# Kernel tuning notes

Measured on AMD Instinct MI355X. Metric: run time of the kernel, lower is better.

## Reference

```python
import jax, jax.numpy as jnp
import numpy as np
from jax import lax

N, CIN, COUT, T, V, S = 64, 64, 64, 256, 25, 3
REL = CIN // 8  # 8, per __init__ branch for in_channels=64


def setup_inputs() -> dict:
    key = jax.random.key(0)
    ks = jax.random.split(key, 22)
    rn = lambda i, shape, s=0.05: jax.random.normal(ks[i], shape, jnp.float32) * s
    return dict(
        x=jax.random.normal(ks[0], (N, CIN, T, V), jnp.float32),
        A=rn(1, (S, V, V), 0.2),                 # adaptive PA parameter
        alpha=jnp.asarray(0.1, jnp.float32),     # unit_gcn alpha (scalar)
        w1=rn(2, (S, REL, CIN)), b1=rn(3, (S, REL)),
        w2=rn(4, (S, REL, CIN)), b2=rn(5, (S, REL)),
        w3=rn(6, (S, COUT, CIN)), b3=rn(7, (S, COUT)),
        w4=rn(8, (S, COUT, REL)), b4=rn(9, (S, COUT)),
        pm_w1=rn(10, (S, REL, 2 * REL)), pm_b1=rn(11, (S, REL)),
        pm_w2=rn(12, (S, REL, REL)), pm_b2=rn(13, (S, REL)),
        dw_w=rn(14, (S, REL, 1, 3, 3)),          # depthwise 3x3, groups=REL
        proj_w=rn(15, (S, COUT, REL)),           # aux_proj, no bias
        beta=rn(16, (S,), 0.01), gamma=rn(17, (S,), 0.01),
        bn_w=jnp.ones((COUT,), jnp.float32), bn_b=jnp.zeros((COUT,), jnp.float32),
    )


def _sorgc(x, Ai, alpha, w1, b1, w2, b2, w3, b3, w4, b4,
           pw1, pb1, pw2, pb2, dww, pjw, beta, gamma):
    # x: (N, C, T, V)
    xm = x.mean(axis=2)                                            # (N,C,V) -- 1x1 conv is linear, so conv then mean == mean then conv
    x1 = jnp.einsum('ncv,rc->nrv', xm, w1) + b1[:, None]           # (N,R,V)
    x2 = jnp.einsum('ncv,rc->nrv', xm, w2) + b2[:, None]
    x3 = jnp.einsum('nctv,oc->notv', x, w3) + b3[:, None, None]    # (N,O,T,V)
    q1 = jnp.tanh(x1[:, :, :, None] - x2[:, :, None, :])           # (N,R,V,V)
    psi = jnp.broadcast_to(x2[:, :, :, None], q1.shape)
    phi = jnp.broadcast_to(x2[:, :, None, :], q1.shape)
    pair = jnp.concatenate([psi, phi], axis=1)                     # (N,2R,V,V)
    h = jax.nn.relu(jnp.einsum('npuv,rp->nruv', pair, pw1) + pb1[:, None, None])
    q2 = jnp.einsum('npuv,rp->nruv', h, pw2) + pb2[:, None, None]
    q_all = q1 + gamma * q2
    R = (jnp.einsum('nruv,or->nouv', q_all, w4) + b4[:, None, None]) * alpha + Ai[None, None]
    # aux branch: depthwise 3x3 conv -> avgpool3x3 (count_include_pad) -> tanh -> 1x1 proj
    Ra = lax.conv_general_dilated(q1, dww, (1, 1), [(1, 1), (1, 1)],
                                  dimension_numbers=('NCHW', 'OIHW', 'NCHW'),
                                  feature_group_count=q1.shape[1])
    Ra = lax.reduce_window(Ra, 0.0, lax.add, (1, 1, 3, 3), (1, 1, 1, 1),
                           [(0, 0), (0, 0), (1, 1), (1, 1)]) / 9.0
    Ra = jnp.tanh(Ra)
    Ra = jnp.einsum('nruv,or->nouv', Ra, pjw)                      # (N,O,V,V)
    R = R + beta * Ra
    return jnp.einsum('ncuv,nctv->nctu', R, x3)                    # (N,O,T,V)


def reference(x, A, alpha, w1, b1, w2, b2, w3, b3, w4, b4,
              pm_w1, pm_b1, pm_w2, pm_b2, dw_w, proj_w, beta, gamma, bn_w, bn_b):
    y = None
    for i in range(S):
        z = _sorgc(x, A[i], alpha, w1[i], b1[i], w2[i], b2[i], w3[i], b3[i],
                   w4[i], b4[i], pm_w1[i], pm_b1[i], pm_w2[i], pm_b2[i],
                   dw_w[i], proj_w[i], beta[i], gamma[i])
        y = z if y is None else y + z
    # BatchNorm2d (training-mode batch statistics), eps=1e-5
    mu = y.mean(axis=(0, 2, 3), keepdims=True)
    var = y.var(axis=(0, 2, 3), keepdims=True)
    y = (y - mu) * lax.rsqrt(var + 1e-5) * bn_w[None, :, None, None] + bn_b[None, :, None, None]
    y = y + x  # residual (in_channels == out_channels -> identity down)
    return jax.nn.relu(y)
```

## Files before the change

### kernel.cpp

```cpp
#include <hip/hip_runtime.h>


#define WS_R_BYTE   409600

typedef __attribute__((ext_vector_type(8))) short bf16x8;
typedef __attribute__((ext_vector_type(4))) float f32x4;

typedef __attribute__((address_space(1))) unsigned int uint_g;
typedef __attribute__((address_space(3))) unsigned int uint_l;

static __device__ __forceinline__ unsigned short f2bf(float f) {
    unsigned int u = __float_as_uint(f);
    u += 0x7fff + ((u >> 16) & 1);
    return (unsigned short)(u >> 16);
}
static __device__ __forceinline__ float bf2f(unsigned short s) {
    return __uint_as_float(((unsigned int)s) << 16);
}
static __device__ __forceinline__ void gload_lds16(const void* g, void* l) {
    __builtin_amdgcn_global_load_lds((const uint_g*)g, (uint_l*)l, 16, 0, 0);
}

__global__ __launch_bounds__(256) void k_xm(const float* __restrict__ x,
                                            float* __restrict__ ws) {
    __shared__ float sm[6400];
    __shared__ float part[200];
    const int tid = threadIdx.x;
    const int n = blockIdx.x >> 6, c = blockIdx.x & 63;
    const float4* p = (const float4*)(x + (unsigned)(n * 64 + c) * 6400u);
    float4* s4 = (float4*)sm;
    for (int i = tid; i < 1600; i += 256) s4[i] = p[i];
    __syncthreads();
    if (tid < 200) {
        int v = tid % 25, g = tid / 25;
        float s = 0.f;
        for (int tt = 0; tt < 32; tt++) s += sm[(g * 32 + tt) * 25 + v];
        part[tid] = s;
    }
    __syncthreads();
    if (tid < 25) {
        float s = 0.f;
        #pragma unroll
        for (int g = 0; g < 8; g++) s += part[g * 25 + tid];
        ws[n * 1600 + c * 25 + tid] = s * (1.f / 256.f);
    }
}

__global__ __launch_bounds__(512) void k_small(
    const float* __restrict__ ws, unsigned short* __restrict__ Rg,
    const float* __restrict__ A, const float* __restrict__ alphap,
    const float* __restrict__ w1, const float* __restrict__ b1,
    const float* __restrict__ w2, const float* __restrict__ b2,
    const float* __restrict__ w4, const float* __restrict__ b4,
    const float* __restrict__ pw1, const float* __restrict__ pb1,
    const float* __restrict__ pw2, const float* __restrict__ pb2,
    const float* __restrict__ dww, const float* __restrict__ pjw,
    const float* __restrict__ beta, const float* __restrict__ gamma) {
    __shared__ float sm[15000];
    const int tid = threadIdx.x;
    const int s = blockIdx.x >> 6;
    const int n = blockIdx.x & 63;
    const float alpha = alphap[0];
    const float gam = gamma[s], bet = beta[s];

    for (int i = tid; i < 1600; i += 512) sm[5000 + i] = ws[n * 1600 + i];
    __syncthreads();

    for (int i = tid; i < 400; i += 512) {
        int half = i / 200, j = i % 200;
        int r = j / 25, k = j % 25;
        const float* w = (half ? w2 : w1) + (s * 8 + r) * 64;
        float acc = (half ? b2 : b1)[s * 8 + r];
        for (int c = 0; c < 64; c++) acc += w[c] * sm[5000 + c * 25 + k];
        sm[6600 + i] = acc;
    }
    __syncthreads();

    for (int i = tid; i < 5400; i += 512) {
        if (i < 5000) {
            int r = i / 625, uv = i % 625, u = uv / 25, v = uv % 25;
            sm[i] = tanhf(sm[6600 + r * 25 + u] - sm[6800 + r * 25 + v]);
        } else {
            int i2 = i - 5000;
            int half = i2 / 200, j = i2 % 200;
            int r = j / 25, k = j % 25;
            float acc = 0.f;
            for (int p = 0; p < 8; p++)
                acc += pw1[(s * 8 + r) * 16 + half * 8 + p] * sm[6800 + p * 25 + k];
            sm[7000 + i2] = acc;
        }
    }
    __syncthreads();

    for (int i = tid; i < 5000; i += 512) {
        int r = i / 625, uv = i % 625, u = uv / 25, v = uv % 25;
        float t = sm[7000 + r * 25 + u] + sm[7200 + r * 25 + v] + pb1[s * 8 + r];
        sm[10000 + i] = t > 0.f ? t : 0.f;
    }
    __syncthreads();

    for (int i = tid; i < 5000; i += 512) {
        int r = i / 625, uv = i % 625;
        float q2 = pb2[s * 8 + r];
        for (int p = 0; p < 8; p++)
            q2 += pw2[(s * 8 + r) * 8 + p] * sm[10000 + p * 625 + uv];
        sm[5000 + i] = sm[i] + gam * q2;
    }
    __syncthreads();

    for (int i = tid; i < 5000; i += 512) {
        int r = i / 625, uv = i % 625, u = uv / 25, v = uv % 25;
        float acc = 0.f;
        for (int di = 0; di < 3; di++) {
            int uu = u + di - 1;
            if (uu < 0 || uu > 24) continue;
            for (int dj = 0; dj < 3; dj++) {
                int vv = v + dj - 1;
                if (vv < 0 || vv > 24) continue;
                acc += sm[r * 625 + uu * 25 + vv] * dww[(s * 8 + r) * 9 + di * 3 + dj];
            }
        }
        sm[10000 + i] = acc;
    }
    __syncthreads();

    for (int i = tid; i < 5000; i += 512) {
        int r = i / 625, uv = i % 625, u = uv / 25, v = uv % 25;
        float acc = 0.f;
        for (int di = 0; di < 3; di++) {
            int uu = u + di - 1;
            if (uu < 0 || uu > 24) continue;
            for (int dj = 0; dj < 3; dj++) {
                int vv = v + dj - 1;
                if (vv < 0 || vv > 24) continue;
                acc += sm[10000 + r * 625 + uu * 25 + vv];
            }
        }
        sm[i] = tanhf(acc * (1.f / 9.f));
    }
    __syncthreads();

    unsigned short* Rb = Rg + (unsigned)(s * 64 + n) * 44800u;
    for (int i = tid; i < 44800; i += 512) {
        int o, vv, uu;
        if (i < 43008) {
            int vg = i / 5376, rem = i % 5376;
            o = rem / 84;
            int j = rem % 84;
            vv = vg * 3 + j / 28;
            uu = j % 28;
        } else {
            int rem = i - 43008;
            o = rem / 28;
            vv = 24;
            uu = rem % 28;
        }
        unsigned short val = 0;
        if (uu < 25) {
            int quv = uu * 25 + vv;
            float mn = b4[s * 64 + o], aux = 0.f;
            for (int r = 0; r < 8; r++) {
                mn  += w4[(s * 64 + o) * 8 + r] * sm[5000 + r * 625 + quv];
                aux += pjw[(s * 64 + o) * 8 + r] * sm[r * 625 + quv];
            }
            val = f2bf(mn * alpha + A[s * 625 + quv] + bet * aux);
        }
        Rb[i] = val;
    }
}

__global__ __launch_bounds__(256, 2) void k_main(
    const float* __restrict__ x, const float* __restrict__ w3,
    const float* __restrict__ b3, const unsigned short* __restrict__ Rg,
    float* __restrict__ out, float* __restrict__ bnacc) {
    __shared__ __align__(16) unsigned char smem[73728];
    unsigned short* xb = (unsigned short*)smem;
    unsigned char* RsBase = smem + 51200;

    const int tid  = threadIdx.x;
    const int blk  = ((int)blockIdx.x & 7) * 128 + ((int)blockIdx.x >> 3);
    const int n    = blk >> 4;
    const int t0   = (blk & 15) * 16;
    const int lane = tid & 63;
    const int w    = tid >> 6;
    const int ln15 = lane & 15;
    const int q    = lane >> 4;
    const int og   = w * 16 + ln15;

    const unsigned short* Rn0 = Rg;

    {
        const char* src = (const char*)Rg + (size_t)((0 * 64 + n) * 44800) * 2;
        unsigned char* dst = RsBase;
        for (int j = w; j < 11; j += 4)
            gload_lds16(src + j * 1024 + (lane << 4), dst + j * 1024);
    }

    {
        const float* xbase = x + n * 409600 + t0 * 25;
        #pragma unroll 5
        for (int k = 0; k < 25; k++) {
            int i  = tid + k * 256;
            int tv = i % 400;
            int cq = i / 400;
            const float* p = xbase + cq * 4 * 6400 + tv;
            ushort4 h;
            h.x = f2bf(p[0]); h.y = f2bf(p[6400]);
            h.z = f2bf(p[12800]); h.w = f2bf(p[19200]);
            int addr = tv * 64 + (((cq >> 1) ^ (tv & 7)) << 3) + ((cq & 1) << 2);
            *(ushort4*)&xb[addr] = h;
        }
    }
    __syncthreads();

    float yacc[25][4];
    #pragma unroll
    for (int u = 0; u < 25; u++)
        #pragma unroll
        for (int r = 0; r < 4; r++) yacc[u][r] = 0.f;

    int buf = 0;
    for (int s = 0; s < 3; s++) {
        bf16x8 bfr[2];
        {
            const float* wp = w3 + (s * 64 + og) * 64;
            #pragma unroll
            for (int ks = 0; ks < 2; ks++)
                #pragma unroll
                for (int j = 0; j < 8; j++)
                    bfr[ks][j] = (short)f2bf(wp[ks * 32 + q * 8 + j]);
        }
        const float bias = b3[s * 64 + og];

        for (int vg = 0; vg < 9; vg++) {
            {
                int ns = s, nvg = vg + 1;
                if (nvg == 9) { ns = s + 1; nvg = 0; }
                if (ns < 3) {
                    const char* src = (const char*)Rg +
                        (size_t)((ns * 64 + n) * 44800 + nvg * 5376) * 2;
                    unsigned char* dst = RsBase + (buf ^ 1) * 11264;
                    const int rounds = (nvg < 8) ? 11 : 4;
                    for (int j = w; j < rounds; j += 4)
                        gload_lds16(src + j * 1024 + (lane << 4), dst + j * 1024);
                }
            }

            const unsigned short* RsB = (const unsigned short*)(RsBase + buf * 11264);
            const int nv = (vg < 8) ? 3 : 1;

            f32x4 c[3];
            #pragma unroll
            for (int iv = 0; iv < 3; iv++) {
                if (iv >= nv) break;
                const int v   = vg * 3 + iv;
                const int row = ln15 * 25 + v;
                const int sw  = row & 7;
                bf16x8 a0 = *(const bf16x8*)&xb[row * 64 + ((q ^ sw) << 3)];
                bf16x8 a1 = *(const bf16x8*)&xb[row * 64 + (((4 + q) ^ sw) << 3)];
                f32x4 cc; cc[0] = bias; cc[1] = bias; cc[2] = bias; cc[3] = bias;
                cc = __builtin_amdgcn_mfma_f32_16x16x32_bf16(a0, bfr[0], cc, 0, 0, 0);
                cc = __builtin_amdgcn_mfma_f32_16x16x32_bf16(a1, bfr[1], cc, 0, 0, 0);
                c[iv] = cc;
            }
            #pragma unroll
            for (int iv = 0; iv < 3; iv++) {
                if (iv >= nv) break;
                const unsigned short* rr = (vg < 8) ? &RsB[og * 84 + iv * 28]
                                                    : &RsB[og * 28];
                f32x4 cc = c[iv];
                #pragma unroll
                for (int ug = 0; ug < 6; ug++) {
                    ushort4 r4 = *(const ushort4*)(rr + ug * 4);
                    float f0 = bf2f(r4.x), f1 = bf2f(r4.y);
                    float f2 = bf2f(r4.z), f3 = bf2f(r4.w);
                    #pragma unroll
                    for (int r = 0; r < 4; r++) {
                        yacc[ug * 4 + 0][r] += f0 * cc[r];
                        yacc[ug * 4 + 1][r] += f1 * cc[r];
                        yacc[ug * 4 + 2][r] += f2 * cc[r];
                        yacc[ug * 4 + 3][r] += f3 * cc[r];
                    }
                }
                float f24 = bf2f(rr[24]);
                #pragma unroll
                for (int r = 0; r < 4; r++) yacc[24][r] += f24 * cc[r];
            }

            __syncthreads();
            buf ^= 1;
        }
    }

    float* op = out + (n * 64 + og) * 6400 + t0 * 25;
    float s1 = 0.f, s2 = 0.f;
    #pragma unroll
    for (int r = 0; r < 4; r++) {
        float* opr = op + (q * 4 + r) * 25;
        #pragma unroll
        for (int u = 0; u < 25; u++) {
            float vv = yacc[u][r];
            opr[u] = vv;
            s1 += vv; s2 += vv * vv;
        }
    }
    s1 += __shfl_xor(s1, 16); s1 += __shfl_xor(s1, 32);
    s2 += __shfl_xor(s2, 16); s2 += __shfl_xor(s2, 32);
    if (q == 0) {
        atomicAdd(&bnacc[og * 16], s1);
        atomicAdd(&bnacc[1024 + og * 16], s2);
    }
}

__global__ __launch_bounds__(256) void k_final(
    float* __restrict__ out, const float* __restrict__ x,
    const float* __restrict__ bnacc,
    const float* __restrict__ bnw, const float* __restrict__ bnb) {
    const int idx4 = blockIdx.x * 256 + threadIdx.x;
    const int o = (idx4 / 1600) & 63;
    const float cnt = 1.f / 409600.f;
    float mean = bnacc[o * 16] * cnt;
    float var = bnacc[1024 + o * 16] * cnt - mean * mean;
    float inv = rsqrtf(var + 1e-5f);
    float sc = bnw[o] * inv;
    float sh = bnb[o] - mean * sc;
    float4 y = ((const float4*)out)[idx4];
    float4 xv = ((const float4*)x)[idx4];
    y.x = fmaxf(y.x * sc + sh + xv.x, 0.f);
    y.y = fmaxf(y.y * sc + sh + xv.y, 0.f);
    y.z = fmaxf(y.z * sc + sh + xv.z, 0.f);
    y.w = fmaxf(y.w * sc + sh + xv.w, 0.f);
    ((float4*)out)[idx4] = y;
}

extern "C" void kernel_launch(void* const* d_in, const int* in_sizes, int n_in,
                              void* d_out, int out_size, void* d_ws, size_t ws_size,
                              hipStream_t stream) {
    const float* x     = (const float*)d_in[0];
    const float* A     = (const float*)d_in[1];
    const float* alpha = (const float*)d_in[2];
    const float* w1    = (const float*)d_in[3];
    const float* b1    = (const float*)d_in[4];
    const float* w2    = (const float*)d_in[5];
    const float* b2    = (const float*)d_in[6];
    const float* w3    = (const float*)d_in[7];
    const float* b3    = (const float*)d_in[8];
    const float* w4    = (const float*)d_in[9];
    const float* b4    = (const float*)d_in[10];
    const float* pw1   = (const float*)d_in[11];
    const float* pb1   = (const float*)d_in[12];
    const float* pw2   = (const float*)d_in[13];
    const float* pb2   = (const float*)d_in[14];
    const float* dww   = (const float*)d_in[15];
    const float* pjw   = (const float*)d_in[16];
    const float* beta  = (const float*)d_in[17];
    const float* gamma = (const float*)d_in[18];
    const float* bnw   = (const float*)d_in[19];
    const float* bnb   = (const float*)d_in[20];
    float* out = (float*)d_out;
    float* ws  = (float*)d_ws;
    unsigned short* wsR = (unsigned short*)((char*)d_ws + WS_R_BYTE);
    float* wsBN = ws;

    k_xm<<<4096, 256, 0, stream>>>(x, ws);
    k_small<<<192, 512, 0, stream>>>(ws, wsR, A, alpha, w1, b1, w2, b2,
                                     w4, b4, pw1, pb1, pw2, pb2, dww, pjw,
                                     beta, gamma);
    hipMemsetAsync(wsBN, 0, 8192, stream);
    k_main<<<1024, 256, 0, stream>>>(x, w3, b3, wsR, out, wsBN);
    k_final<<<25600, 256, 0, stream>>>(out, x, wsBN, bnw, bnb);
}
```

Baseline: 434.0 us.

## Merge last v-groups, use packed f32x2 FMAs, fold memset, double k_final work

Several changes at once. The R layout is reorganised so the final v-group covers four columns (21-24) instead of a separate single-column group, which cuts the main-loop iterations and barriers from 9 to 8 per s. The accumulator becomes f32x2 vectors so the compiler can emit packed FMA instructions. The BN accumulator memset moves into k_xm (block 0) at a separate workspace offset, which removes a launch, and k_final processes two float4s per thread. The costs are larger LDS buffers, which may affect occupancy, and a zeroing step that depends on kernel ordering.

```diff
diff --git a/kernel.cpp b/kernel.cpp
--- a/kernel.cpp
+++ b/kernel.cpp
@@ -2,9 +2,11 @@
 
 
 #define WS_R_BYTE   409600
+#define WS_BN_BYTE  17612800
 
 typedef __attribute__((ext_vector_type(8))) short bf16x8;
 typedef __attribute__((ext_vector_type(4))) float f32x4;
+typedef __attribute__((ext_vector_type(2))) float f32x2;
 
 typedef __attribute__((address_space(1))) unsigned int uint_g;
 typedef __attribute__((address_space(3))) unsigned int uint_l;
@@ -22,10 +24,14 @@
 }
 
 __global__ __launch_bounds__(256) void k_xm(const float* __restrict__ x,
-                                            float* __restrict__ ws) {
+                                            float* __restrict__ ws,
+                                            float* __restrict__ bnacc) {
     __shared__ float sm[6400];
     __shared__ float part[200];
     const int tid = threadIdx.x;
+    if (blockIdx.x == 0) {
+        for (int i = tid; i < 2048; i += 256) bnacc[i] = 0.f;
+    }
     const int n = blockIdx.x >> 6, c = blockIdx.x & 63;
     const float4* p = (const float4*)(x + (unsigned)(n * 64 + c) * 6400u);
     float4* s4 = (float4*)sm;
@@ -143,17 +149,18 @@
     unsigned short* Rb = Rg + (unsigned)(s * 64 + n) * 44800u;
     for (int i = tid; i < 44800; i += 512) {
         int o, vv, uu;
-        if (i < 43008) {
+        if (i < 37632) {
             int vg = i / 5376, rem = i % 5376;
             o = rem / 84;
             int j = rem % 84;
             vv = vg * 3 + j / 28;
             uu = j % 28;
         } else {
-            int rem = i - 43008;
-            o = rem / 28;
-            vv = 24;
-            uu = rem % 28;
+            int rem = i - 37632;
+            o = rem / 112;
+            int j = rem % 112;
+            vv = 21 + j / 28;
+            uu = j % 28;
         }
         unsigned short val = 0;
         if (uu < 25) {
@@ -173,7 +180,7 @@
     const float* __restrict__ x, const float* __restrict__ w3,
     const float* __restrict__ b3, const unsigned short* __restrict__ Rg,
     float* __restrict__ out, float* __restrict__ bnacc) {
-    __shared__ __align__(16) unsigned char smem[73728];
+    __shared__ __align__(16) unsigned char smem[79872];
     unsigned short* xb = (unsigned short*)smem;
     unsigned char* RsBase = smem + 51200;
 
@@ -187,10 +194,8 @@
     const int q    = lane >> 4;
     const int og   = w * 16 + ln15;
 
-    const unsigned short* Rn0 = Rg;
-
     {
-        const char* src = (const char*)Rg + (size_t)((0 * 64 + n) * 44800) * 2;
+        const char* src = (const char*)Rg + (size_t)(n * 44800) * 2;
         unsigned char* dst = RsBase;
         for (int j = w; j < 11; j += 4)
             gload_lds16(src + j * 1024 + (lane << 4), dst + j * 1024);
@@ -213,11 +218,12 @@
     }
     __syncthreads();
 
-    float yacc[25][4];
+    f32x2 yacc[25][2];
     #pragma unroll
-    for (int u = 0; u < 25; u++)
-        #pragma unroll
-        for (int r = 0; r < 4; r++) yacc[u][r] = 0.f;
+    for (int u = 0; u < 25; u++) {
+        yacc[u][0] = (f32x2){0.f, 0.f};
+        yacc[u][1] = (f32x2){0.f, 0.f};
+    }
 
     int buf = 0;
     for (int s = 0; s < 3; s++) {
@@ -232,26 +238,27 @@
         }
         const float bias = b3[s * 64 + og];
 
-        for (int vg = 0; vg < 9; vg++) {
+        for (int vg = 0; vg < 8; vg++) {
             {
                 int ns = s, nvg = vg + 1;
-                if (nvg == 9) { ns = s + 1; nvg = 0; }
+                if (nvg == 8) { ns = s + 1; nvg = 0; }
                 if (ns < 3) {
                     const char* src = (const char*)Rg +
                         (size_t)((ns * 64 + n) * 44800 + nvg * 5376) * 2;
-                    unsigned char* dst = RsBase + (buf ^ 1) * 11264;
-                    const int rounds = (nvg < 8) ? 11 : 4;
+                    unsigned char* dst = RsBase + (buf ^ 1) * 14336;
+                    const int rounds = (nvg < 7) ? 11 : 14;
                     for (int j = w; j < rounds; j += 4)
                         gload_lds16(src + j * 1024 + (lane << 4), dst + j * 1024);
                 }
             }
 
-            const unsigned short* RsB = (const unsigned short*)(RsBase + buf * 11264);
-            const int nv = (vg < 8) ? 3 : 1;
-
-            f32x4 c[3];
+            const unsigned short* RsB = (const unsigned short*)(RsBase + buf * 14336);
+            const int nv = (vg < 7) ? 3 : 4;
+            const int rowstride = (vg < 7) ? 84 : 112;
+
+            f32x4 c[4];
             #pragma unroll
-            for (int iv = 0; iv < 3; iv++) {
+            for (int iv = 0; iv < 4; iv++) {
                 if (iv >= nv) break;
                 const int v   = vg * 3 + iv;
                 const int row = ln15 * 25 + v;
@@ -264,27 +271,25 @@
                 c[iv] = cc;
             }
             #pragma unroll
-            for (int iv = 0; iv < 3; iv++) {
+            for (int iv = 0; iv < 4; iv++) {
                 if (iv >= nv) break;
-                const unsigned short* rr = (vg < 8) ? &RsB[og * 84 + iv * 28]
-                                                    : &RsB[og * 28];
-                f32x4 cc = c[iv];
+                const unsigned short* rr = &RsB[og * rowstride + iv * 28];
+                f32x2 c01, c23;
+                c01[0] = c[iv][0]; c01[1] = c[iv][1];
+                c23[0] = c[iv][2]; c23[1] = c[iv][3];
                 #pragma unroll
                 for (int ug = 0; ug < 6; ug++) {
                     ushort4 r4 = *(const ushort4*)(rr + ug * 4);
                     float f0 = bf2f(r4.x), f1 = bf2f(r4.y);
                     float f2 = bf2f(r4.z), f3 = bf2f(r4.w);
-                    #pragma unroll
-                    for (int r = 0; r < 4; r++) {
-                        yacc[ug * 4 + 0][r] += f0 * cc[r];
-                        yacc[ug * 4 + 1][r] += f1 * cc[r];
-                        yacc[ug * 4 + 2][r] += f2 * cc[r];
-                        yacc[ug * 4 + 3][r] += f3 * cc[r];
-                    }
+                    yacc[ug * 4 + 0][0] += f0 * c01; yacc[ug * 4 + 0][1] += f0 * c23;
+                    yacc[ug * 4 + 1][0] += f1 * c01; yacc[ug * 4 + 1][1] += f1 * c23;
+                    yacc[ug * 4 + 2][0] += f2 * c01; yacc[ug * 4 + 2][1] += f2 * c23;
+                    yacc[ug * 4 + 3][0] += f3 * c01; yacc[ug * 4 + 3][1] += f3 * c23;
                 }
                 float f24 = bf2f(rr[24]);
-                #pragma unroll
-                for (int r = 0; r < 4; r++) yacc[24][r] += f24 * cc[r];
+                yacc[24][0] += f24 * c01;
+                yacc[24][1] += f24 * c23;
             }
 
             __syncthreads();
@@ -297,9 +302,10 @@
     #pragma unroll
     for (int r = 0; r < 4; r++) {
         float* opr = op + (q * 4 + r) * 25;
+        const int h = r >> 1, jj = r & 1;
         #pragma unroll
         for (int u = 0; u < 25; u++) {
-            float vv = yacc[u][r];
+            float vv = yacc[u][h][jj];
             opr[u] = vv;
             s1 += vv; s2 += vv * vv;
         }
@@ -316,21 +322,25 @@
     float* __restrict__ out, const float* __restrict__ x,
     const float* __restrict__ bnacc,
     const float* __restrict__ bnw, const float* __restrict__ bnb) {
-    const int idx4 = blockIdx.x * 256 + threadIdx.x;
-    const int o = (idx4 / 1600) & 63;
+    const int base = blockIdx.x * 512 + threadIdx.x;
     const float cnt = 1.f / 409600.f;
-    float mean = bnacc[o * 16] * cnt;
-    float var = bnacc[1024 + o * 16] * cnt - mean * mean;
-    float inv = rsqrtf(var + 1e-5f);
-    float sc = bnw[o] * inv;
-    float sh = bnb[o] - mean * sc;
-    float4 y = ((const float4*)out)[idx4];
-    float4 xv = ((const float4*)x)[idx4];
-    y.x = fmaxf(y.x * sc + sh + xv.x, 0.f);
-    y.y = fmaxf(y.y * sc + sh + xv.y, 0.f);
-    y.z = fmaxf(y.z * sc + sh + xv.z, 0.f);
-    y.w = fmaxf(y.w * sc + sh + xv.w, 0.f);
-    ((float4*)out)[idx4] = y;
+    #pragma unroll
+    for (int e = 0; e < 2; e++) {
+        const int idx4 = base + e * 256;
+        const int o = (idx4 / 1600) & 63;
+        float mean = bnacc[o * 16] * cnt;
+        float var = bnacc[1024 + o * 16] * cnt - mean * mean;
+        float inv = rsqrtf(var + 1e-5f);
+        float sc = bnw[o] * inv;
+        float sh = bnb[o] - mean * sc;
+        float4 y = ((const float4*)out)[idx4];
+        float4 xv = ((const float4*)x)[idx4];
+        y.x = fmaxf(y.x * sc + sh + xv.x, 0.f);
+        y.y = fmaxf(y.y * sc + sh + xv.y, 0.f);
+        y.z = fmaxf(y.z * sc + sh + xv.z, 0.f);
+        y.w = fmaxf(y.w * sc + sh + xv.w, 0.f);
+        ((float4*)out)[idx4] = y;
+    }
 }
 
 extern "C" void kernel_launch(void* const* d_in, const int* in_sizes, int n_in,
@@ -360,13 +370,12 @@
     float* out = (float*)d_out;
     float* ws  = (float*)d_ws;
     unsigned short* wsR = (unsigned short*)((char*)d_ws + WS_R_BYTE);
-    float* wsBN = ws;
-
-    k_xm<<<4096, 256, 0, stream>>>(x, ws);
+    float* wsBN = (float*)((char*)d_ws + WS_BN_BYTE);
+
+    k_xm<<<4096, 256, 0, stream>>>(x, ws, wsBN);
     k_small<<<192, 512, 0, stream>>>(ws, wsR, A, alpha, w1, b1, w2, b2,
                                      w4, b4, pw1, pb1, pw2, pb2, dww, pjw,
                                      beta, gamma);
-    hipMemsetAsync(wsBN, 0, 8192, stream);
     k_main<<<1024, 256, 0, stream>>>(x, w3, b3, wsR, out, wsBN);
-    k_final<<<25600, 256, 0, stream>>>(out, x, wsBN, bnw, bnb);
-}
+    k_final<<<12800, 256, 0, stream>>>(out, x, wsBN, bnw, bnb);
+}
```

Result: no change. 429.5 us (-1.0%).
